# Kernel tuning notes

Hardware: AMD Instinct MI355X
Metric: run time of the kernel (lower is better)

## Reference

```python
import jax, jax.numpy as jnp
import numpy as np

NUM_BINS = 3
TAIL_BOUND = 1.0


def conv3x3(x, w, b):
    # x: [B,C,H,W], w: [O,I,3,3]
    y = jax.lax.conv_general_dilated(x, w, (1, 1), 'SAME',
                                     dimension_numbers=('NCHW', 'OIHW', 'NCHW'))
    return y + b[None, :, None, None]


def unconstrained_linear_spline(inputs, unnormalized_pdf, tail_bound=TAIL_BOUND):
    # inputs: [B,C,H,W]; unnormalized_pdf: [B,C,H,W,num_bins]
    num_bins = unnormalized_pdf.shape[-1]
    left = bottom = -tail_bound
    right = top = tail_bound
    inside = (inputs >= left) & (inputs <= right)

    x = (inputs - left) / (right - left)  # scale to [0,1]
    pdf = jax.nn.softmax(unnormalized_pdf, axis=-1)
    cdf = jnp.cumsum(pdf, axis=-1)
    cdf = cdf.at[..., -1].set(1.0)
    cdf = jnp.pad(cdf, [(0, 0)] * (cdf.ndim - 1) + [(1, 0)])  # [..., num_bins+1]

    pos = jnp.clip(x, 0.0, 1.0) * num_bins  # clip keeps bin idx valid for outside elems
    bin_idx = jnp.clip(jnp.floor(pos).astype(jnp.int32), 0, num_bins - 1)
    alpha = pos - bin_idx.astype(pos.dtype)

    input_pdfs = jnp.take_along_axis(pdf, bin_idx[..., None], axis=-1)[..., 0]
    out = jnp.take_along_axis(cdf, bin_idx[..., None], axis=-1)[..., 0] + alpha * input_pdfs
    out = jnp.clip(out, 0.0, 1.0)
    lad = jnp.log(input_pdfs) + jnp.log(jnp.asarray(num_bins, pos.dtype))

    out = out * (top - bottom) + bottom
    lad = lad - jnp.log(jnp.asarray(top - bottom, pos.dtype)) + jnp.log(jnp.asarray(right - left, pos.dtype))

    out = jnp.where(inside, out, inputs)       # identity tails
    lad = jnp.where(inside, lad, 0.0)
    return out, lad


def setup_inputs() -> dict:
    key = jax.random.key(0)
    ks = jax.random.split(key, 4)
    B, C, H, W = 32, 64, 64, 64
    hidden = 128
    c_half = C // 2
    c_out = c_half * NUM_BINS
    x = jax.random.normal(ks[0], (B, C, H, W), dtype=jnp.float32)
    objective = jnp.zeros((B,), dtype=jnp.float32)
    W1 = jax.random.normal(ks[1], (hidden, c_half, 3, 3), dtype=jnp.float32) * 0.05
    b1 = jnp.zeros((hidden,), dtype=jnp.float32)
    W2 = jax.random.normal(ks[2], (c_out, hidden, 3, 3), dtype=jnp.float32) * 0.05
    b2 = jnp.zeros((c_out,), dtype=jnp.float32)
    return {'x': x, 'objective': objective, 'W1': W1, 'b1': b1, 'W2': W2, 'b2': b2}


def reference(x, objective, W1, b1, W2, b2):
    identity_split, transform_split = jnp.split(x, 2, axis=1)
    h = jax.nn.relu(conv3x3(identity_split, W1, b1))
    transform_params = conv3x3(h, W2, b2)  # [B, C/2*num_bins, H, W]
    b, c, hh, ww = transform_split.shape
    transform_params = transform_params.reshape(b, c, NUM_BINS, hh, ww).transpose(0, 1, 3, 4, 2)
    transformed, logabsdet = unconstrained_linear_spline(transform_split, transform_params)
    output = jnp.concatenate([identity_split, transformed], axis=1)
    objective_out = objective + jnp.sum(logabsdet.reshape(b, -1), axis=1)
    return output, objective_out
```

## Files before the change

### kernel.cpp

```cpp
#include <hip/hip_runtime.h>

typedef __attribute__((ext_vector_type(8))) __bf16 bf16x8;
typedef __attribute__((ext_vector_type(4))) float f32x4;

__device__ __forceinline__ unsigned short f2bf(float f) {
    unsigned int u = __builtin_bit_cast(unsigned int, f);
    u = (u + 0x7FFFu + ((u >> 16) & 1u)) >> 16;
    return (unsigned short)u;
}

__global__ void __launch_bounds__(256) prep_x1(const float* __restrict__ x,
                                               unsigned short* __restrict__ x1b) {
    int bh = blockIdx.x;
    __shared__ unsigned short lds[64][34];
    int t = threadIdx.x;
    int w = t & 63, c4 = t >> 6;
    const float* xp = x + (size_t)(bh >> 6) * 262144 + (size_t)(bh & 63) * 64;
#pragma unroll
    for (int co = 0; co < 8; ++co) {
        int c = co * 4 + c4;
        lds[w][c] = f2bf(xp[(size_t)c * 4096 + w]);
    }
    __syncthreads();
    int wq = t >> 2, c0 = (t & 3) * 8;
    uint4 v;
    unsigned short* pv = reinterpret_cast<unsigned short*>(&v);
#pragma unroll
    for (int j = 0; j < 8; ++j) pv[j] = lds[wq][c0 + j];
    *reinterpret_cast<uint4*>(x1b + ((size_t)bh * 64 + wq) * 32 + c0) = v;
}

__global__ void __launch_bounds__(256) prep_copy(const float* __restrict__ x,
                                                 const float* __restrict__ obj,
                                                 float* __restrict__ out) {
    unsigned tid = blockIdx.x * 256 + threadIdx.x;
    unsigned b = tid >> 15, r = tid & 32767;
    size_t off = (size_t)b * 65536 + r;
    reinterpret_cast<float4*>(out)[off] = reinterpret_cast<const float4*>(x)[off];
    if (tid < 32) out[8388608 + tid] = obj[tid];
}

__global__ void __launch_bounds__(256) prep_w(const float* __restrict__ W1,
                                              const float* __restrict__ W2,
                                              unsigned short* __restrict__ Wt1,
                                              unsigned short* __restrict__ Wt2) {
    int tid = blockIdx.x * 256 + threadIdx.x;
    if (tid < 36864) {
        int tt = tid % 9, rem = tid / 9;
        int i = rem & 31, o = rem >> 5;
        Wt1[(tt * 128 + o) * 32 + i] = f2bf(W1[tid]);
    }
    if (tid < 110592) {
        int tt = tid % 9, rem = tid / 9;
        int i = rem & 127, o = rem >> 7;
        int kc = i >> 6, ii = i & 63;
        Wt2[(((kc * 9 + tt) * 96 + o) * 64) + ii] = f2bf(W2[tid]);
    }
}

__global__ void __launch_bounds__(256) conv1_relu(const unsigned short* __restrict__ x1b,
                                                  const float* __restrict__ b1,
                                                  const unsigned short* __restrict__ Wt1,
                                                  unsigned short* __restrict__ hbuf) {
    const int LW = 40;
    __shared__ unsigned short sx[6 * 66 * LW];
    int wg = blockIdx.x;
    int b = wg >> 4, h0 = (wg & 15) << 2;
    int t = threadIdx.x;

    if (t < 48) {
        int row = t >> 3, k = t & 7;
        int col = (k & 1) ? 65 : 0, c0 = (k >> 1) * 8;
        *reinterpret_cast<uint4*>(&sx[(row * 66 + col) * LW + c0]) = uint4{0, 0, 0, 0};
    }
#pragma unroll
    for (int j = 0; j < 6; ++j) {
        int idx = j * 256 + t;
        int row = idx >> 8, rem = idx & 255;
        int w = rem >> 2, c0 = (rem & 3) * 8;
        int gh = h0 - 1 + row;
        uint4 v = uint4{0, 0, 0, 0};
        if (gh >= 0 && gh < 64)
            v = *reinterpret_cast<const uint4*>(x1b + (((size_t)b * 64 + gh) * 64 + w) * 32 + c0);
        *reinterpret_cast<uint4*>(&sx[(row * 66 + (w + 1)) * LW + c0]) = v;
    }
    __syncthreads();

    int wid = t >> 6, lane = t & 63;
    int lrow = lane & 15, kgrp = lane >> 4;

    bf16x8 afr[2][9];
#pragma unroll
    for (int m2 = 0; m2 < 2; ++m2) {
        int o = (wid * 2 + m2) * 16 + lrow;
#pragma unroll
        for (int tap = 0; tap < 9; ++tap)
            afr[m2][tap] = *reinterpret_cast<const bf16x8*>(
                Wt1 + (size_t)(tap * 128 + o) * 32 + kgrp * 8);
    }

    for (int nt = 0; nt < 16; ++nt) {
        int r = nt >> 2, ww = ((nt & 3) << 4) + lrow;
        f32x4 acc0 = {0.f, 0.f, 0.f, 0.f}, acc1 = {0.f, 0.f, 0.f, 0.f};
#pragma unroll
        for (int dh = 0; dh < 3; ++dh)
#pragma unroll
            for (int dw = 0; dw < 3; ++dw) {
                int tap = dh * 3 + dw;
                bf16x8 bfr = *reinterpret_cast<const bf16x8*>(
                    &sx[((r + dh) * 66 + ww + dw) * LW + kgrp * 8]);
                acc0 = __builtin_amdgcn_mfma_f32_16x16x32_bf16(afr[0][tap], bfr, acc0, 0, 0, 0);
                acc1 = __builtin_amdgcn_mfma_f32_16x16x32_bf16(afr[1][tap], bfr, acc1, 0, 0, 0);
            }
        int hh = h0 + r;
        size_t obase = (((size_t)b * 64 + hh) * 64 + ww) * 128;
#pragma unroll
        for (int m2 = 0; m2 < 2; ++m2) {
            f32x4 a = (m2 == 0) ? acc0 : acc1;
            int o0 = (wid * 2 + m2) * 16 + kgrp * 4;
            unsigned short r4[4];
#pragma unroll
            for (int j = 0; j < 4; ++j) {
                float v = a[j] + b1[o0 + j];
                r4[j] = f2bf(fmaxf(v, 0.f));
            }
            uint2 pk;
            pk.x = (unsigned)r4[0] | ((unsigned)r4[1] << 16);
            pk.y = (unsigned)r4[2] | ((unsigned)r4[3] << 16);
            *reinterpret_cast<uint2*>(hbuf + obase + o0) = pk;
        }
    }
}

__global__ void __launch_bounds__(512) conv2_spline(const unsigned short* __restrict__ hbuf,
                                                    const float* __restrict__ b2,
                                                    const unsigned short* __restrict__ Wt2,
                                                    const float* __restrict__ x,
                                                    float* __restrict__ out) {
    const int LWA = 72;
    const int LWW = 72;
    __shared__ unsigned short sa[6 * 66 * LWA];
    __shared__ unsigned short sw[96 * LWW];
    __shared__ float red[8];
    float* pm = reinterpret_cast<float*>(sa);

    int raw = blockIdx.x;
    int wg = (raw & 7) * 64 + (raw >> 3);
    int b = wg >> 4, h0 = (wg & 15) << 2;
    int t = threadIdx.x;
    int wid = t >> 6, lane = t & 63;
    int lrow = lane & 15, kgrp = lane >> 4;
    int mgrp = wid >> 2, ngrp = wid & 3;
    int mb = mgrp * 3;

    int wo_a = t >> 3, wk_a = t & 7;
    int wdst_a = wo_a * LWW + wk_a * 8;
    int wsrc_a = wo_a * 64 + wk_a * 8;
    int f2 = 512 + t;
    int wo_b = f2 >> 3, wk_b = f2 & 7;
    int wdst_b = wo_b * LWW + wk_b * 8;
    int wsrc_b = wo_b * 64 + wk_b * 8;

    f32x4 acc[3][4];
#pragma unroll
    for (int i = 0; i < 3; ++i)
#pragma unroll
        for (int j = 0; j < 4; ++j) acc[i][j] = f32x4{0.f, 0.f, 0.f, 0.f};

    {
        uint4 v1 = *reinterpret_cast<const uint4*>(Wt2 + wsrc_a);
        *reinterpret_cast<uint4*>(&sw[wdst_a]) = v1;
        if (t < 256) {
            uint4 v2 = *reinterpret_cast<const uint4*>(Wt2 + wsrc_b);
            *reinterpret_cast<uint4*>(&sw[wdst_b]) = v2;
        }
    }

    for (int kc2 = 0; kc2 < 2; ++kc2) {
#pragma unroll
        for (int j = 0; j < 6; ++j) {
            int idx = j * 512 + t;
            int row = idx >> 9, rem = idx & 511;
            int w = rem >> 3, c0 = (rem & 7) * 8;
            int gh = h0 - 1 + row;
            uint4 v = uint4{0, 0, 0, 0};
            if (gh >= 0 && gh < 64)
                v = *reinterpret_cast<const uint4*>(
                    hbuf + (((size_t)b * 64 + gh) * 64 + w) * 128 + kc2 * 64 + c0);
            *reinterpret_cast<uint4*>(&sa[(row * 66 + (w + 1)) * LWA + c0]) = v;
        }
        if (t < 96) {
            int row = t >> 4, k = t & 15;
            int col = (k & 1) ? 65 : 0, c0 = (k >> 1) * 8;
            *reinterpret_cast<uint4*>(&sa[(row * 66 + col) * LWA + c0]) = uint4{0, 0, 0, 0};
        }
        __syncthreads();

        for (int tap = 0; tap < 9; ++tap) {
            int s = kc2 * 9 + tap;
            uint4 v1, v2;
            if (s < 17) {
                const unsigned short* wsrc = Wt2 + (size_t)(s + 1) * 6144;
                v1 = *reinterpret_cast<const uint4*>(wsrc + wsrc_a);
                if (t < 256) v2 = *reinterpret_cast<const uint4*>(wsrc + wsrc_b);
            }

            int dh = tap / 3, dw = tap % 3;
            bf16x8 wfr[3][2];
#pragma unroll
            for (int mi = 0; mi < 3; ++mi) {
                int o = (mb + mi) * 16 + lrow;
                wfr[mi][0] = *reinterpret_cast<const bf16x8*>(&sw[o * LWW + kgrp * 8]);
                wfr[mi][1] = *reinterpret_cast<const bf16x8*>(&sw[o * LWW + 32 + kgrp * 8]);
            }
#pragma unroll
            for (int ni = 0; ni < 4; ++ni) {
                int nt = ngrp * 4 + ni;
                int rr = nt >> 2, wcol = (nt & 3) * 16 + lrow;
                int base = ((rr + dh) * 66 + wcol + dw) * LWA;
                bf16x8 a0 = *reinterpret_cast<const bf16x8*>(&sa[base + kgrp * 8]);
                bf16x8 a1 = *reinterpret_cast<const bf16x8*>(&sa[base + 32 + kgrp * 8]);
#pragma unroll
                for (int mi = 0; mi < 3; ++mi) {
                    acc[mi][ni] = __builtin_amdgcn_mfma_f32_16x16x32_bf16(wfr[mi][0], a0, acc[mi][ni], 0, 0, 0);
                    acc[mi][ni] = __builtin_amdgcn_mfma_f32_16x16x32_bf16(wfr[mi][1], a1, acc[mi][ni], 0, 0, 0);
                }
            }
            __syncthreads();
            if (s < 17) {
                *reinterpret_cast<uint4*>(&sw[wdst_a]) = v1;
                if (t < 256) *reinterpret_cast<uint4*>(&sw[wdst_b]) = v2;
            }
            __syncthreads();
        }
    }

    float lad_acc = 0.f;
    for (int half = 0; half < 2; ++half) {
        __syncthreads();
        if ((ngrp >> 1) == half) {
#pragma unroll
            for (int mi = 0; mi < 3; ++mi) {
                int o0 = (mb + mi) * 16 + kgrp * 4;
                float bb0 = b2[o0], bb1 = b2[o0 + 1], bb2 = b2[o0 + 2], bb3 = b2[o0 + 3];
#pragma unroll
                for (int ni = 0; ni < 4; ++ni) {
                    int p = (ngrp & 1) * 64 + ni * 16 + lrow;
                    f32x4 v = acc[mi][ni];
                    pm[p * 101 + o0]     = v[0] + bb0;
                    pm[p * 101 + o0 + 1] = v[1] + bb1;
                    pm[p * 101 + o0 + 2] = v[2] + bb2;
                    pm[p * 101 + o0 + 3] = v[3] + bb3;
                }
            }
        }
        __syncthreads();
#pragma unroll 4
        for (int it = 0; it < 8; ++it) {
            int idx = it * 512 + t;
            int c = idx >> 7, p = idx & 127;
            int pos = half * 128 + p;
            int pb = p * 101 + 3 * c;
            float u0 = pm[pb];
            float u1 = pm[pb + 1];
            float u2 = pm[pb + 2];
            size_t gpos = (size_t)(b * 64 + 32 + c) * 4096 + (size_t)(h0 + (pos >> 6)) * 64 + (pos & 63);
            float xin = x[gpos];
            float mx = fmaxf(u0, fmaxf(u1, u2));
            float e0 = __expf(u0 - mx), e1 = __expf(u1 - mx), e2 = __expf(u2 - mx);
            float s = e0 + e1 + e2;
            float inv = 1.0f / s;
            float pos01 = fminf(fmaxf((xin + 1.f) * 0.5f, 0.f), 1.f) * 3.f;
            int bin = (int)pos01; bin = bin > 2 ? 2 : bin;
            float alpha = pos01 - (float)bin;
            float eb = (bin == 0) ? e0 : ((bin == 1) ? e1 : e2);
            float cb = (bin == 0) ? 0.f : ((bin == 1) ? e0 : (e0 + e1));
            float pk = eb * inv;
            float outv = cb * inv + alpha * pk;
            outv = fminf(fmaxf(outv, 0.f), 1.f) * 2.f - 1.f;
            float lad = __logf(pk) + 1.09861228866810969f;
            bool inside = (xin >= -1.f) && (xin <= 1.f);
            if (!inside) { outv = xin; lad = 0.f; }
            out[gpos] = outv;
            lad_acc += lad;
        }
    }
#pragma unroll
    for (int off = 32; off > 0; off >>= 1)
        lad_acc += __shfl_down(lad_acc, off, 64);
    if (lane == 0) red[wid] = lad_acc;
    __syncthreads();
    if (t == 0) {
        float s = 0.f;
#pragma unroll
        for (int i = 0; i < 8; ++i) s += red[i];
        atomicAdd(out + 8388608 + b, s);
    }
}

extern "C" void kernel_launch(void* const* d_in, const int* in_sizes, int n_in,
                              void* d_out, int out_size, void* d_ws, size_t ws_size,
                              hipStream_t stream) {
    const float* x   = (const float*)d_in[0];
    const float* obj = (const float*)d_in[1];
    const float* W1  = (const float*)d_in[2];
    const float* b1  = (const float*)d_in[3];
    const float* W2  = (const float*)d_in[4];
    const float* b2  = (const float*)d_in[5];
    float* out = (float*)d_out;
    char* ws = (char*)d_ws;

    unsigned short* x1b  = (unsigned short*)ws;
    unsigned short* hbuf = (unsigned short*)(ws + 8388608);
    unsigned short* Wt1  = (unsigned short*)(ws + 8388608 + 33554432);
    unsigned short* Wt2  = (unsigned short*)(ws + 8388608 + 33554432 + 73728);

    hipLaunchKernelGGL(prep_x1,      dim3(2048), dim3(256), 0, stream, x, x1b);
    hipLaunchKernelGGL(prep_copy,    dim3(4096), dim3(256), 0, stream, x, obj, out);
    hipLaunchKernelGGL(prep_w,       dim3(432),  dim3(256), 0, stream, W1, W2, Wt1, Wt2);
    hipLaunchKernelGGL(conv1_relu,   dim3(512),  dim3(256), 0, stream, x1b, b1, Wt1, hbuf);
    hipLaunchKernelGGL(conv2_spline, dim3(512),  dim3(512), 0, stream, hbuf, b2, Wt2, x, out);
}
```

Baseline: 77.55 us.

## Fuse bf16 input staging and identity-half copy into conv1 kernel

Removes the separate prep_x1 and prep_copy kernels. conv1 now reads fp32 x directly, converts it to bf16 into LDS including halo rows, and also copies its slab of the identity channels to the output. This saves two launches and the round trip through the intermediate x1b buffer. In exchange, each block re-reads two halo rows of fp32 input and does scalar strided LDS stores, which may add bank conflicts and lengthen the conv1 prologue.

```diff
diff --git a/kernel.cpp b/kernel.cpp
--- a/kernel.cpp
+++ b/kernel.cpp
@@ -7,37 +7,6 @@
     unsigned int u = __builtin_bit_cast(unsigned int, f);
     u = (u + 0x7FFFu + ((u >> 16) & 1u)) >> 16;
     return (unsigned short)u;
-}
-
-__global__ void __launch_bounds__(256) prep_x1(const float* __restrict__ x,
-                                               unsigned short* __restrict__ x1b) {
-    int bh = blockIdx.x;
-    __shared__ unsigned short lds[64][34];
-    int t = threadIdx.x;
-    int w = t & 63, c4 = t >> 6;
-    const float* xp = x + (size_t)(bh >> 6) * 262144 + (size_t)(bh & 63) * 64;
-#pragma unroll
-    for (int co = 0; co < 8; ++co) {
-        int c = co * 4 + c4;
-        lds[w][c] = f2bf(xp[(size_t)c * 4096 + w]);
-    }
-    __syncthreads();
-    int wq = t >> 2, c0 = (t & 3) * 8;
-    uint4 v;
-    unsigned short* pv = reinterpret_cast<unsigned short*>(&v);
-#pragma unroll
-    for (int j = 0; j < 8; ++j) pv[j] = lds[wq][c0 + j];
-    *reinterpret_cast<uint4*>(x1b + ((size_t)bh * 64 + wq) * 32 + c0) = v;
-}
-
-__global__ void __launch_bounds__(256) prep_copy(const float* __restrict__ x,
-                                                 const float* __restrict__ obj,
-                                                 float* __restrict__ out) {
-    unsigned tid = blockIdx.x * 256 + threadIdx.x;
-    unsigned b = tid >> 15, r = tid & 32767;
-    size_t off = (size_t)b * 65536 + r;
-    reinterpret_cast<float4*>(out)[off] = reinterpret_cast<const float4*>(x)[off];
-    if (tid < 32) out[8388608 + tid] = obj[tid];
 }
 
 __global__ void __launch_bounds__(256) prep_w(const float* __restrict__ W1,
@@ -58,31 +27,54 @@
     }
 }
 
-__global__ void __launch_bounds__(256) conv1_relu(const unsigned short* __restrict__ x1b,
-                                                  const float* __restrict__ b1,
-                                                  const unsigned short* __restrict__ Wt1,
-                                                  unsigned short* __restrict__ hbuf) {
+__global__ void __launch_bounds__(256) conv1_fused(const float* __restrict__ x,
+                                                   const float* __restrict__ obj,
+                                                   const float* __restrict__ b1,
+                                                   const unsigned short* __restrict__ Wt1,
+                                                   unsigned short* __restrict__ hbuf,
+                                                   float* __restrict__ out) {
     const int LW = 40;
     __shared__ unsigned short sx[6 * 66 * LW];
     int wg = blockIdx.x;
     int b = wg >> 4, h0 = (wg & 15) << 2;
     int t = threadIdx.x;
 
+#pragma unroll
+    for (int j = 0; j < 8; ++j) {
+        int idx = j * 256 + t;
+        int c = idx >> 6, row = (idx >> 4) & 3, w4 = idx & 15;
+        size_t off = (((size_t)b * 64 + c) * 64 + (h0 + row)) * 16 + w4;
+        reinterpret_cast<float4*>(out)[off] =
+            reinterpret_cast<const float4*>(x)[off];
+    }
+    if (wg == 0 && t < 32) out[8388608 + t] = obj[t];
+
     if (t < 48) {
         int row = t >> 3, k = t & 7;
         int col = (k & 1) ? 65 : 0, c0 = (k >> 1) * 8;
         *reinterpret_cast<uint4*>(&sx[(row * 66 + col) * LW + c0]) = uint4{0, 0, 0, 0};
     }
-#pragma unroll
-    for (int j = 0; j < 6; ++j) {
-        int idx = j * 256 + t;
-        int row = idx >> 8, rem = idx & 255;
-        int w = rem >> 2, c0 = (rem & 3) * 8;
-        int gh = h0 - 1 + row;
-        uint4 v = uint4{0, 0, 0, 0};
-        if (gh >= 0 && gh < 64)
-            v = *reinterpret_cast<const uint4*>(x1b + (((size_t)b * 64 + gh) * 64 + w) * 32 + c0);
-        *reinterpret_cast<uint4*>(&sx[(row * 66 + (w + 1)) * LW + c0]) = v;
+    {
+        int w = t & 63, c4 = t >> 6;
+        const float* xb = x + (size_t)b * 262144;
+#pragma unroll
+        for (int row = 0; row < 6; ++row) {
+            int gh = h0 - 1 + row;
+            if (gh >= 0 && gh < 64) {
+                const float* xr = xb + (size_t)gh * 64;
+#pragma unroll
+                for (int co = 0; co < 8; ++co) {
+                    int c = co * 4 + c4;
+                    sx[(row * 66 + w + 1) * LW + c] = f2bf(xr[(size_t)c * 4096 + w]);
+                }
+            } else {
+#pragma unroll
+                for (int co = 0; co < 8; ++co) {
+                    int c = co * 4 + c4;
+                    sx[(row * 66 + w + 1) * LW + c] = 0;
+                }
+            }
+        }
     }
     __syncthreads();
 
@@ -310,14 +302,11 @@
     float* out = (float*)d_out;
     char* ws = (char*)d_ws;
 
-    unsigned short* x1b  = (unsigned short*)ws;
-    unsigned short* hbuf = (unsigned short*)(ws + 8388608);
-    unsigned short* Wt1  = (unsigned short*)(ws + 8388608 + 33554432);
-    unsigned short* Wt2  = (unsigned short*)(ws + 8388608 + 33554432 + 73728);
-
-    hipLaunchKernelGGL(prep_x1,      dim3(2048), dim3(256), 0, stream, x, x1b);
-    hipLaunchKernelGGL(prep_copy,    dim3(4096), dim3(256), 0, stream, x, obj, out);
-    hipLaunchKernelGGL(prep_w,       dim3(432),  dim3(256), 0, stream, W1, W2, Wt1, Wt2);
-    hipLaunchKernelGGL(conv1_relu,   dim3(512),  dim3(256), 0, stream, x1b, b1, Wt1, hbuf);
-    hipLaunchKernelGGL(conv2_spline, dim3(512),  dim3(512), 0, stream, hbuf, b2, Wt2, x, out);
-}
+    unsigned short* hbuf = (unsigned short*)ws;
+    unsigned short* Wt1  = (unsigned short*)(ws + 33554432);
+    unsigned short* Wt2  = (unsigned short*)(ws + 33554432 + 73728);
+
+    hipLaunchKernelGGL(prep_w,       dim3(432), dim3(256), 0, stream, W1, W2, Wt1, Wt2);
+    hipLaunchKernelGGL(conv1_fused,  dim3(512), dim3(256), 0, stream, x, obj, b1, Wt1, hbuf, out);
+    hipLaunchKernelGGL(conv2_spline, dim3(512), dim3(512), 0, stream, hbuf, b2, Wt2, x, out);
+}
```

Result: faster. 73.85 us (-4.8%).
